# Kernel tuning notes

Hardware: AMD Instinct MI355X
Metric: run time of the kernel (lower is better)

## Reference

```python
import jax, jax.numpy as jnp
import numpy as np

NEG_INF = -9e15
ALPHA = 2.0  # LeakyReLU negative slope from init (alpha=2)


def setup_inputs() -> dict:
    key = jax.random.key(0)
    k1, k2, k3, k4 = jax.random.split(key, 4)
    B, N, Fin, Fout = 8, 2048, 256, 128
    x = jax.random.normal(k1, (B, N, Fin), dtype=jnp.float32)
    adj = jax.random.randint(k2, (B, N, N), 0, 2, dtype=jnp.int32)
    # xavier_uniform with gain=1.414
    def xavier(k, shape, gain=1.414):
        fan_in, fan_out = shape[0], shape[1]
        bound = gain * np.sqrt(6.0 / (fan_in + fan_out))
        return jax.random.uniform(k, shape, jnp.float32, -bound, bound)
    W = xavier(k3, (Fin, Fout))
    a = xavier(k4, (2 * Fout, 1))
    return {"x": x, "adj": adj, "W": W, "a": a}


def reference(x, adj, W, a):
    # Wh: [B, N, Fout]
    Wh = jnp.matmul(x, W)
    Fout = W.shape[1]
    a1 = a[:Fout, 0]   # [Fout]
    a2 = a[Fout:, 0]   # [Fout]
    f1 = jnp.einsum('bnf,f->bn', Wh, a1)  # [B, N]
    f2 = jnp.einsum('bnf,f->bn', Wh, a2)  # [B, N]
    e = f1[:, :, None] + f2[:, None, :]   # [B, N, N]
    e = jnp.where(e >= 0, e, ALPHA * e)   # leaky relu, slope 2
    e = jnp.where(adj > 0, e, NEG_INF)
    attention = jax.nn.softmax(e, axis=2)
    # dropout: eval mode (no-op)
    h_prime = jnp.matmul(attention, Wh)   # [B, N, Fout]
    # concat=True -> elu
    return jnp.where(h_prime > 0, h_prime, jnp.expm1(h_prime))
```

## Files before the change

### kernel.cpp

```cpp
#include <hip/hip_runtime.h>
#include <hip/hip_bf16.h>
#include <math.h>

constexpr int B_   = 8;
constexpr int N_   = 2048;
constexpr int FIN  = 256;
constexpr int FOUT = 128;

constexpr int CH  = 512;
constexpr int NCH = N_ / CH;
constexpr int PR  = CH + 8;
constexpr int XR  = FIN + 8;
constexpr int TR  = 40;

typedef __attribute__((ext_vector_type(8))) short bf16x8;
typedef __attribute__((ext_vector_type(4))) float f32x4;
typedef __attribute__((ext_vector_type(4))) int   i32x4;

static __device__ __forceinline__ unsigned short f2bf(float f) {
    __hip_bfloat16 h = __float2bfloat16(f);
    return *reinterpret_cast<unsigned short*>(&h);
}
static __device__ __forceinline__ i32x4 ntload4(const int* p) {
    return __builtin_nontemporal_load((const i32x4*)p);
}

__global__ __launch_bounds__(256) void k0_wt(const float* __restrict__ W,
                                             unsigned short* __restrict__ Wt) {
    Wt[blockIdx.x * FIN + threadIdx.x] = f2bf(W[threadIdx.x * FOUT + blockIdx.x]);
}

__global__ __launch_bounds__(256) void kf_ka_pack(
        const float* __restrict__ x,
        const unsigned short* __restrict__ Wt,
        const float* __restrict__ a,
        const int* __restrict__ adj,
        unsigned short* __restrict__ Whf,
        float* __restrict__ f1,
        float* __restrict__ f2,
        unsigned long long* __restrict__ maskW) {
    __shared__ unsigned short xs[32 * XR];
    __shared__ float as[2 * FOUT];
    __shared__ float fred[2][4][32];

    const int beta = blockIdx.x;
    const int tid  = threadIdx.x;

    if (beta % 5 != 0) {
        const int pid  = beta - beta / 5 - 1;
        const int lane = tid & 63, wv = tid >> 6;
        const int gbase = pid * 64 + wv * 16;
        for (int t0 = 0; t0 < 16; t0 += 4) {
            i32x4 vv[4];
#pragma unroll
            for (int u = 0; u < 4; ++u)
                vv[u] = ntload4(adj + (size_t)(gbase + t0 + u) * 256 + 4 * lane);
#pragma unroll
            for (int u = 0; u < 4; ++u) {
                const int g = gbase + t0 + u;
                unsigned long long b0 = __ballot(vv[u][0] > 0);
                unsigned long long b1 = __ballot(vv[u][1] > 0);
                unsigned long long b2 = __ballot(vv[u][2] > 0);
                unsigned long long b3 = __ballot(vv[u][3] > 0);
                if (lane < 4) {
                    unsigned long long w = (lane == 0) ? b0
                                         : (lane == 1) ? b1
                                         : (lane == 2) ? b2 : b3;
                    maskW[(size_t)4 * g + lane] = w;
                }
            }
        }
        return;
    }

    const int j0 = (beta / 5) * 32;
    const int b  = j0 >> 11;
    const int jb = j0 & (N_ - 1);

    if (tid < 2 * FOUT) as[tid] = a[tid];
    {
        const float4* xsrc = (const float4*)(x + (size_t)j0 * FIN);
#pragma unroll
        for (int t = 0; t < 8; ++t) {
            const int idx = tid + t * 256;
            float4 v = xsrc[idx];
            const int row = idx >> 6, c4 = idx & 63;
            ushort4 u;
            u.x = f2bf(v.x); u.y = f2bf(v.y); u.z = f2bf(v.z); u.w = f2bf(v.w);
            *(ushort4*)&xs[row * XR + c4 * 4] = u;
        }
    }
    __syncthreads();

    const int wave = tid >> 6, lane = tid & 63;
    const int quad = lane >> 4, l16 = lane & 15;

    f32x4 acc[2][2];
#pragma unroll
    for (int aa = 0; aa < 2; ++aa)
#pragma unroll
        for (int nn = 0; nn < 2; ++nn) acc[aa][nn] = {0.f, 0.f, 0.f, 0.f};

    const unsigned short* wtA0 = Wt + (size_t)(32 * wave + l16) * FIN;
    const unsigned short* wtA1 = wtA0 + 16 * FIN;
#pragma unroll
    for (int ks = 0; ks < FIN / 32; ++ks) {
        const int kof = ks * 32 + quad * 8;
        bf16x8 af0 = *(const bf16x8*)&wtA0[kof];
        bf16x8 af1 = *(const bf16x8*)&wtA1[kof];
        bf16x8 bf0 = *(const bf16x8*)&xs[l16 * XR + kof];
        bf16x8 bf1 = *(const bf16x8*)&xs[(16 + l16) * XR + kof];
        acc[0][0] = __builtin_amdgcn_mfma_f32_16x16x32_bf16(af0, bf0, acc[0][0], 0, 0, 0);
        acc[0][1] = __builtin_amdgcn_mfma_f32_16x16x32_bf16(af0, bf1, acc[0][1], 0, 0, 0);
        acc[1][0] = __builtin_amdgcn_mfma_f32_16x16x32_bf16(af1, bf0, acc[1][0], 0, 0, 0);
        acc[1][1] = __builtin_amdgcn_mfma_f32_16x16x32_bf16(af1, bf1, acc[1][1], 0, 0, 0);
    }
    __syncthreads();

    unsigned short* T = xs;
    float pf[2][2] = {{0.f, 0.f}, {0.f, 0.f}};
#pragma unroll
    for (int aa = 0; aa < 2; ++aa)
#pragma unroll
        for (int nn = 0; nn < 2; ++nn)
#pragma unroll
            for (int r = 0; r < 4; ++r) {
                const int d = 32 * wave + 16 * aa + 4 * quad + r;
                const float v = acc[aa][nn][r];
                T[d * TR + nn * 16 + l16] = f2bf(v);
                pf[0][nn] += v * as[d];
                pf[1][nn] += v * as[FOUT + d];
            }
#pragma unroll
    for (int ff = 0; ff < 2; ++ff)
#pragma unroll
        for (int nn = 0; nn < 2; ++nn) {
            float v = pf[ff][nn];
            v += __shfl_xor(v, 16);
            v += __shfl_xor(v, 32);
            pf[ff][nn] = v;
        }
    if (quad == 0) {
#pragma unroll
        for (int ff = 0; ff < 2; ++ff)
#pragma unroll
            for (int nn = 0; nn < 2; ++nn)
                fred[ff][wave][nn * 16 + l16] = pf[ff][nn];
    }
    __syncthreads();

    unsigned short* dstW = Whf + (size_t)(b * 8) * 256 * 128;
    const int jb8 = jb >> 3;
#pragma unroll
    for (int it = 0; it < 2; ++it) {
        const int i   = it * 256 + tid;
        const int n16 = i & 15, q = (i >> 4) & 3, nt = i >> 6;
        bf16x8 v = *(const bf16x8*)&T[(nt * 16 + n16) * TR + q * 8];
        *(bf16x8*)&dstW[((size_t)nt * 256 + jb8 + q) * 128 + n16 * 8] = v;
    }
    if (tid < 64) {
        const int ff = tid >> 5, j32 = tid & 31;
        const float s = fred[ff][0][j32] + fred[ff][1][j32] +
                        fred[ff][2][j32] + fred[ff][3][j32];
        (ff ? f2 : f1)[(size_t)b * N_ + jb + j32] = s;
    }
}

__global__ __launch_bounds__(512, 4) void kb_attn(const unsigned long long* __restrict__ maskW,
                                                  const unsigned short* __restrict__ Whf,
                                                  const float* __restrict__ f1,
                                                  const float* __restrict__ f2,
                                                  float* __restrict__ out) {
    __shared__ unsigned short p[2][16 * PR];
    __shared__ float rsum[16];

    const int tid  = threadIdx.x;
    const int b    = blockIdx.x & 7;
    const int i0   = (blockIdx.x >> 3) * 16;
    const int wave = tid >> 6, lane = tid & 63;
    const int quad = lane >> 4, l16 = lane & 15;

    const f32x4* f2b4 = (const f32x4*)(f2 + (size_t)b * N_);

    float f1r[2], s_run[2];
#pragma unroll
    for (int rr = 0; rr < 2; ++rr) {
        f1r[rr]   = f1[(size_t)b * N_ + i0 + wave * 2 + rr];
        s_run[rr] = 0.f;
    }

    f32x4 acc = {0.f, 0.f, 0.f, 0.f};
    const unsigned short* wAll =
        Whf + ((size_t)(b * 8 + wave) * 256) * 128 + quad * 128 + l16 * 8;

    auto PROCESS = [&](int c) {
        unsigned short* pb = &p[c & 1][0];
        const f32x4 fva = f2b4[c * (CH / 4) + lane];
        const f32x4 fvb = f2b4[c * (CH / 4) + 64 + lane];
#pragma unroll
        for (int rr = 0; rr < 2; ++rr) {
            const int ti = wave * 2 + rr;
            const float f1i = f1r[rr];
            const size_t gbase =
                (((size_t)b * N_ + (size_t)(i0 + ti)) * N_ + (size_t)c * CH) >> 8;
            const unsigned long long* mw = maskW + 4 * gbase;
            const unsigned long long m00 = mw[0], m01 = mw[1];
            const unsigned long long m02 = mw[2], m03 = mw[3];
            const unsigned long long m10 = mw[4], m11 = mw[5];
            const unsigned long long m12 = mw[6], m13 = mw[7];

            float e[8];
            e[0] = f1i + fva[0]; e[1] = f1i + fva[1];
            e[2] = f1i + fva[2]; e[3] = f1i + fva[3];
            e[4] = f1i + fvb[0]; e[5] = f1i + fvb[1];
            e[6] = f1i + fvb[2]; e[7] = f1i + fvb[3];
#pragma unroll
            for (int q = 0; q < 8; ++q) e[q] = (e[q] >= 0.f) ? e[q] : 2.f * e[q];

            float pv[8];
            pv[0] = ((m00 >> lane) & 1ull) ? __expf(e[0]) : 0.f;
            pv[1] = ((m01 >> lane) & 1ull) ? __expf(e[1]) : 0.f;
            pv[2] = ((m02 >> lane) & 1ull) ? __expf(e[2]) : 0.f;
            pv[3] = ((m03 >> lane) & 1ull) ? __expf(e[3]) : 0.f;
            pv[4] = ((m10 >> lane) & 1ull) ? __expf(e[4]) : 0.f;
            pv[5] = ((m11 >> lane) & 1ull) ? __expf(e[5]) : 0.f;
            pv[6] = ((m12 >> lane) & 1ull) ? __expf(e[6]) : 0.f;
            pv[7] = ((m13 >> lane) & 1ull) ? __expf(e[7]) : 0.f;

            s_run[rr] += ((pv[0] + pv[1]) + (pv[2] + pv[3])) +
                         ((pv[4] + pv[5]) + (pv[6] + pv[7]));

            ushort4 u0, u1;
            u0.x = f2bf(pv[0]); u0.y = f2bf(pv[1]);
            u0.z = f2bf(pv[2]); u0.w = f2bf(pv[3]);
            u1.x = f2bf(pv[4]); u1.y = f2bf(pv[5]);
            u1.z = f2bf(pv[6]); u1.w = f2bf(pv[7]);
            *(ushort4*)&pb[ti * PR + 4 * lane]       = u0;
            *(ushort4*)&pb[ti * PR + 256 + 4 * lane] = u1;
        }
    };

    PROCESS(0);
    __syncthreads();

    for (int c = 0; c < NCH; ++c) {
        if (c + 1 < NCH) {
            PROCESS(c + 1);
        } else {
#pragma unroll
            for (int rr = 0; rr < 2; ++rr) {
                float s = s_run[rr];
#pragma unroll
                for (int o = 32; o; o >>= 1) s += __shfl_xor(s, o);
                if (lane == 0) rsum[wave * 2 + rr] = s;
            }
        }

        const unsigned short* wBc = wAll + (size_t)c * (64 * 128);
        const unsigned short* pA = &p[c & 1][l16 * PR];
#pragma unroll
        for (int ks = 0; ks < CH / 32; ++ks) {
            bf16x8 bfr = *(const bf16x8*)&wBc[ks * 512];
            bf16x8 afr = *(const bf16x8*)&pA[ks * 32 + quad * 8];
            acc = __builtin_amdgcn_mfma_f32_16x16x32_bf16(afr, bfr, acc,
                                                          0, 0, 0);
        }
        __syncthreads();
    }

#pragma unroll
    for (int r = 0; r < 4; ++r) {
        const int m = quad * 4 + r;
        const float inv = 1.f / rsum[m];
        float v = acc[r] * inv;
        v = (v > 0.f) ? v : expm1f(v);
        out[((size_t)b * N_ + i0 + m) * FOUT + wave * 16 + l16] = v;
    }
}

extern "C" void kernel_launch(void* const* d_in, const int* in_sizes, int n_in,
                              void* d_out, int out_size, void* d_ws, size_t ws_size,
                              hipStream_t stream) {
    const float* x   = (const float*)d_in[0];
    const int*   adj = (const int*)d_in[1];
    const float* W   = (const float*)d_in[2];
    const float* a   = (const float*)d_in[3];
    float* out = (float*)d_out;

    unsigned short* Whf = (unsigned short*)d_ws;
    unsigned short* Wt  = Whf + (size_t)B_ * FOUT * N_;
    float* f1 = (float*)(Wt + (size_t)FOUT * FIN);
    float* f2 = f1 + (size_t)B_ * N_;
    unsigned long long* maskW = (unsigned long long*)(f2 + (size_t)B_ * N_);

    hipLaunchKernelGGL(k0_wt, dim3(FOUT), dim3(FIN), 0, stream, W, Wt);
    hipLaunchKernelGGL(kf_ka_pack, dim3(512 + 2048), dim3(256), 0, stream,
                       x, Wt, a, adj, Whf, f1, f2, maskW);
    hipLaunchKernelGGL(kb_attn, dim3(B_ * N_ / 16), dim3(512), 0, stream,
                       maskW, Whf, f1, f2, out);
}
```

Before: 236.0 us.

## Process 32 query rows per attention block to reuse Wh fragments across two MFMAs

The attention kernel now handles 32 rows per block instead of 16. Each wave computes four rows of softmax numerators and issues two MFMAs per loaded Wh fragment. This halves the Wh reads from global/L2 per output row and halves the grid size. In exchange it doubles LDS for the P buffer (about 66KB), adds register pressure, and leaves fewer blocks to fill the GPU.

```diff
diff --git a/kernel.cpp b/kernel.cpp
--- a/kernel.cpp
+++ b/kernel.cpp
@@ -9,7 +9,8 @@
 
 constexpr int CH  = 512;
 constexpr int NCH = N_ / CH;
-constexpr int PR  = CH + 8;
+constexpr int PR  = 520;
+constexpr int KR  = 32;
 constexpr int XR  = FIN + 8;
 constexpr int TR  = 40;
 
@@ -171,25 +172,26 @@
                                                   const float* __restrict__ f1,
                                                   const float* __restrict__ f2,
                                                   float* __restrict__ out) {
-    __shared__ unsigned short p[2][16 * PR];
-    __shared__ float rsum[16];
+    __shared__ unsigned short p[2][KR * PR];
+    __shared__ float rsum[KR];
 
     const int tid  = threadIdx.x;
     const int b    = blockIdx.x & 7;
-    const int i0   = (blockIdx.x >> 3) * 16;
+    const int i0   = (blockIdx.x >> 3) * KR;
     const int wave = tid >> 6, lane = tid & 63;
     const int quad = lane >> 4, l16 = lane & 15;
 
     const f32x4* f2b4 = (const f32x4*)(f2 + (size_t)b * N_);
 
-    float f1r[2], s_run[2];
-#pragma unroll
-    for (int rr = 0; rr < 2; ++rr) {
-        f1r[rr]   = f1[(size_t)b * N_ + i0 + wave * 2 + rr];
+    float f1r[4], s_run[4];
+#pragma unroll
+    for (int rr = 0; rr < 4; ++rr) {
+        f1r[rr]   = f1[(size_t)b * N_ + i0 + wave * 4 + rr];
         s_run[rr] = 0.f;
     }
 
-    f32x4 acc = {0.f, 0.f, 0.f, 0.f};
+    f32x4 acc0 = {0.f, 0.f, 0.f, 0.f};
+    f32x4 acc1 = {0.f, 0.f, 0.f, 0.f};
     const unsigned short* wAll =
         Whf + ((size_t)(b * 8 + wave) * 256) * 128 + quad * 128 + l16 * 8;
 
@@ -198,8 +200,8 @@
         const f32x4 fva = f2b4[c * (CH / 4) + lane];
         const f32x4 fvb = f2b4[c * (CH / 4) + 64 + lane];
 #pragma unroll
-        for (int rr = 0; rr < 2; ++rr) {
-            const int ti = wave * 2 + rr;
+        for (int rr = 0; rr < 4; ++rr) {
+            const int ti = wave * 4 + rr;
             const float f1i = f1r[rr];
             const size_t gbase =
                 (((size_t)b * N_ + (size_t)(i0 + ti)) * N_ + (size_t)c * CH) >> 8;
@@ -248,33 +250,41 @@
             PROCESS(c + 1);
         } else {
 #pragma unroll
-            for (int rr = 0; rr < 2; ++rr) {
+            for (int rr = 0; rr < 4; ++rr) {
                 float s = s_run[rr];
 #pragma unroll
                 for (int o = 32; o; o >>= 1) s += __shfl_xor(s, o);
-                if (lane == 0) rsum[wave * 2 + rr] = s;
+                if (lane == 0) rsum[wave * 4 + rr] = s;
             }
         }
 
         const unsigned short* wBc = wAll + (size_t)c * (64 * 128);
-        const unsigned short* pA = &p[c & 1][l16 * PR];
+        const unsigned short* pA0 = &p[c & 1][l16 * PR];
+        const unsigned short* pA1 = &p[c & 1][(16 + l16) * PR];
 #pragma unroll
         for (int ks = 0; ks < CH / 32; ++ks) {
-            bf16x8 bfr = *(const bf16x8*)&wBc[ks * 512];
-            bf16x8 afr = *(const bf16x8*)&pA[ks * 32 + quad * 8];
-            acc = __builtin_amdgcn_mfma_f32_16x16x32_bf16(afr, bfr, acc,
-                                                          0, 0, 0);
+            bf16x8 bfr  = *(const bf16x8*)&wBc[ks * 512];
+            bf16x8 afr0 = *(const bf16x8*)&pA0[ks * 32 + quad * 8];
+            bf16x8 afr1 = *(const bf16x8*)&pA1[ks * 32 + quad * 8];
+            acc0 = __builtin_amdgcn_mfma_f32_16x16x32_bf16(afr0, bfr, acc0,
+                                                           0, 0, 0);
+            acc1 = __builtin_amdgcn_mfma_f32_16x16x32_bf16(afr1, bfr, acc1,
+                                                           0, 0, 0);
         }
         __syncthreads();
     }
 
 #pragma unroll
-    for (int r = 0; r < 4; ++r) {
-        const int m = quad * 4 + r;
-        const float inv = 1.f / rsum[m];
-        float v = acc[r] * inv;
-        v = (v > 0.f) ? v : expm1f(v);
-        out[((size_t)b * N_ + i0 + m) * FOUT + wave * 16 + l16] = v;
+    for (int t = 0; t < 2; ++t) {
+        const f32x4 accT = t ? acc1 : acc0;
+#pragma unroll
+        for (int r = 0; r < 4; ++r) {
+            const int m = t * 16 + quad * 4 + r;
+            const float inv = 1.f / rsum[m];
+            float v = accT[r] * inv;
+            v = (v > 0.f) ? v : expm1f(v);
+            out[((size_t)b * N_ + i0 + m) * FOUT + wave * 16 + l16] = v;
+        }
     }
 }
 
@@ -296,6 +306,6 @@
     hipLaunchKernelGGL(k0_wt, dim3(FOUT), dim3(FIN), 0, stream, W, Wt);
     hipLaunchKernelGGL(kf_ka_pack, dim3(512 + 2048), dim3(256), 0, stream,
                        x, Wt, a, adj, Whf, f1, f2, maskW);
-    hipLaunchKernelGGL(kb_attn, dim3(B_ * N_ / 16), dim3(512), 0, stream,
+    hipLaunchKernelGGL(kb_attn, dim3(B_ * N_ / KR), dim3(512), 0, stream,
                        maskW, Whf, f1, f2, out);
 }
```

After: 231.2 us (median of 2 runs). 2.0% less time.
